# Performance work log

Hardware: AMD Instinct MI355X
Metric: run time of the kernel (lower is better)

## Reference

```python
import jax, jax.numpy as jnp
import numpy as np

NUM_HEADS = 8
HEAD_DIM = 64
D_MODEL = NUM_HEADS * HEAD_DIM  # 512
B, T = 4, 2048


def setup_inputs() -> dict:
    key = jax.random.key(0)
    k1, k2 = jax.random.split(key)
    x = jax.random.normal(k1, (B, T, D_MODEL), dtype=jnp.float32)
    mask = jnp.ones((B, 1, T, T), dtype=jnp.float32)
    W = jax.random.normal(k2, (D_MODEL, 3 * D_MODEL), dtype=jnp.float32) * (D_MODEL ** -0.5)
    b = jnp.zeros((3 * D_MODEL,), dtype=jnp.float32)
    return {"x": x, "mask": mask, "W": W, "b": b}


def reference(x, mask, W, b):
    batch = x.shape[0]
    # fused QKV projection: [B, T, 3D]
    qkv = jnp.einsum("btd,de->bte", x, W) + b
    # NOTE: faithful to torch reshape [B, T, H, Hd, 3] -> the size-3 axis is innermost
    qkv = qkv.reshape(batch, -1, NUM_HEADS, HEAD_DIM, 3)
    qkv = jnp.transpose(qkv, (4, 0, 2, 1, 3))  # [3, B, H, T, Hd]
    q, k, v = qkv[0], qkv[1], qkv[2]
    logits = jnp.einsum("bhqd,bhkd->bhqk", q, k) / (HEAD_DIM ** 0.5)
    logits = logits + (1.0 - mask) * -10000.0
    w = jax.nn.softmax(logits, axis=-1)
    out = jnp.einsum("bhqk,bhkd->bhqd", w, v)  # [B, H, T, Hd]
    out = jnp.transpose(out, (0, 2, 1, 3)).reshape(batch, -1, NUM_HEADS * HEAD_DIM)
    return out
```

## Files before the change

### kernel.cpp

```cpp
#include <hip/hip_runtime.h>
#include <hip/hip_bf16.h>
#include <stdint.h>

#define B_   4
#define T_   2048
#define H_   8
#define HD_  64
#define DM_  512
#define N3_  1536

typedef short bf_el;
typedef __attribute__((ext_vector_type(8))) bf_el bfrag;
typedef __attribute__((ext_vector_type(4))) float ffrag;

#define SCALE_L2E  0.18033688011112043f
#define MASK_L2E   14426.950408889634f

static __device__ __forceinline__ unsigned short f2bf(float f) {
    union { float f; unsigned int i; } v; v.f = f;
    unsigned int r = v.i + 0x7fff + ((v.i >> 16) & 1);
    return (unsigned short)(r >> 16);
}
static __device__ __forceinline__ unsigned short f2bf_fast(float f) {
    union { float f; unsigned int i; } v; v.f = f;
    return (unsigned short)((v.i + 0x8000u) >> 16);
}

__global__ __launch_bounds__(256) void k_prep(const float* __restrict__ W,
                                              const float* __restrict__ X,
                                              const float* __restrict__ mask,
                                              unsigned short* __restrict__ Wt,
                                              unsigned short* __restrict__ Xb,
                                              int* __restrict__ flags) {
    __shared__ __align__(16) unsigned short Ls[64 * 72];
    const int bid = blockIdx.x;
    const int tid = threadIdx.x;

    if (bid < 512) {
        const int R0 = bid * 16;
        const int mb = R0 >> 11;
        const int q0 = R0 & 2047;
        const int e  = mb * 32 + (q0 >> 6);
        const int wave = tid >> 6, lane = tid & 63;
        unsigned int acc = 0u;
        const float* base = mask + (size_t)R0 * T_ + tid * 8;
#pragma unroll
        for (int rr = 0; rr < 16; ++rr) {
            const uint4 u0 = *(const uint4*)(base + (size_t)rr * T_);
            const uint4 u1 = *(const uint4*)(base + (size_t)rr * T_ + 4);
            acc |= (u0.x ^ 0x3F800000u) | (u0.y ^ 0x3F800000u) |
                   (u0.z ^ 0x3F800000u) | (u0.w ^ 0x3F800000u) |
                   (u1.x ^ 0x3F800000u) | (u1.y ^ 0x3F800000u) |
                   (u1.z ^ 0x3F800000u) | (u1.w ^ 0x3F800000u);
        }
        unsigned long long bal = __ballot(acc != 0u);
        if (lane == 0 && bal != 0ULL) {
#pragma unroll
            for (int j = 0; j < 8; ++j)
                if ((bal >> (8 * j)) & 0xFFULL)
                    atomicOr(&flags[e * 32 + wave * 8 + j], 1);
        }
        return;
    }
    if (bid < 768) {
        const int b2 = bid - 512;
        const float* src = X + (size_t)b2 * 16384;
        unsigned short* dst = Xb + (size_t)b2 * 16384;
#pragma unroll
        for (int j = 0; j < 8; ++j) {
            int idx = j * 512 + tid * 2;
            float4 f0 = *(const float4*)(src + idx * 4);
            float4 f1 = *(const float4*)(src + idx * 4 + 4);
            __align__(16) unsigned short t8[8];
            t8[0] = f2bf_fast(f0.x); t8[1] = f2bf_fast(f0.y);
            t8[2] = f2bf_fast(f0.z); t8[3] = f2bf_fast(f0.w);
            t8[4] = f2bf_fast(f1.x); t8[5] = f2bf_fast(f1.y);
            t8[6] = f2bf_fast(f1.z); t8[7] = f2bf_fast(f1.w);
            *(uint4*)(dst + idx * 4) = *(const uint4*)t8;
        }
        return;
    }
    {
        const int t  = bid - 768;
        const int n0 = (t % 24) * 64;
        const int k0 = (t / 24) * 64;
#pragma unroll
        for (int i = 0; i < 4; ++i) {
            int chunk = tid + i * 256;
            int k = chunk >> 4;
            int c = chunk & 15;
            float4 f = *(const float4*)(W + (size_t)(k0 + k) * N3_ + n0 + c * 4);
            unsigned short* p = Ls + k * 72 + c * 4;
            p[0] = f2bf(f.x); p[1] = f2bf(f.y); p[2] = f2bf(f.z); p[3] = f2bf(f.w);
        }
        __syncthreads();
        const int n = tid >> 2;
        const int g = tid & 3;
        __align__(16) unsigned short tmp[16];
#pragma unroll
        for (int i = 0; i < 16; ++i) tmp[i] = Ls[(g * 16 + i) * 72 + n];
        uint4* dst = (uint4*)(Wt + (size_t)(n0 + n) * DM_ + k0 + g * 16);
        dst[0] = *(const uint4*)(tmp);
        dst[1] = *(const uint4*)(tmp + 8);
    }
}

__global__ __launch_bounds__(256) void k_gemm_qkv(const unsigned short* __restrict__ Xb,
                                                  const unsigned short* __restrict__ Wt,
                                                  const float* __restrict__ bias,
                                                  unsigned short* __restrict__ Qb,
                                                  unsigned short* __restrict__ Kb,
                                                  unsigned short* __restrict__ Vtb) {
    __shared__ __align__(16) unsigned short SH[12800];
    unsigned short* As = SH;
    unsigned short* Bs = SH + 5120;
    unsigned short* Cs = SH;

    const int tid  = threadIdx.x;
    const int wave = tid >> 6;
    const int lane = tid & 63;
    const int quad = lane >> 4;
    const int l16  = lane & 15;
    const int wm = wave >> 1, wn = wave & 1;
    const int h  = blockIdx.x >> 6;
    const int m0 = (blockIdx.x & 63) * 128;
    const int n0 = h * 192;

    float bvv[6];
#pragma unroll
    for (int ni = 0; ni < 6; ++ni) bvv[ni] = bias[n0 + wn * 96 + ni * 16 + l16];

    ffrag acc[4][6];
#pragma unroll
    for (int i = 0; i < 4; ++i)
#pragma unroll
        for (int j = 0; j < 6; ++j) acc[i][j] = (ffrag){0.f, 0.f, 0.f, 0.f};

    for (int kt = 0; kt < 16; ++kt) {
        __syncthreads();
#pragma unroll
        for (int i = 0; i < 2; ++i) {
            int chunk = tid + i * 256;
            int r = chunk >> 2, c = chunk & 3;
            *(uint4*)(As + r * 40 + c * 8) =
                *(const uint4*)(Xb + (size_t)(m0 + r) * DM_ + kt * 32 + c * 8);
        }
#pragma unroll
        for (int i = 0; i < 3; ++i) {
            int chunk = tid + i * 256;
            int r = chunk >> 2, c = chunk & 3;
            *(uint4*)(Bs + r * 40 + c * 8) =
                *(const uint4*)(Wt + (size_t)(n0 + r) * DM_ + kt * 32 + c * 8);
        }
        __syncthreads();
        bfrag af[4], bfr[6];
#pragma unroll
        for (int mi = 0; mi < 4; ++mi)
            af[mi] = *(const bfrag*)(As + (wm * 64 + mi * 16 + l16) * 40 + quad * 8);
#pragma unroll
        for (int ni = 0; ni < 6; ++ni)
            bfr[ni] = *(const bfrag*)(Bs + (wn * 96 + ni * 16 + l16) * 40 + quad * 8);
#pragma unroll
        for (int mi = 0; mi < 4; ++mi)
#pragma unroll
            for (int ni = 0; ni < 6; ++ni)
                acc[mi][ni] = __builtin_amdgcn_mfma_f32_16x16x32_bf16(af[mi], bfr[ni], acc[mi][ni], 0, 0, 0);
    }

    const int b   = m0 >> 11;
    const int tb0 = m0 & 2047;
    const size_t bh = (size_t)(b * 8 + h);
    float cscale[6];
#pragma unroll
    for (int ni = 0; ni < 6; ++ni) {
        int c = wn * 96 + ni * 16 + l16;
        cscale[ni] = (c % 3 == 0) ? SCALE_L2E : 1.0f;
    }
#pragma unroll
    for (int half = 0; half < 2; ++half) {
        __syncthreads();
        if (wm == half) {
#pragma unroll
            for (int mi = 0; mi < 4; ++mi)
#pragma unroll
                for (int ni = 0; ni < 6; ++ni)
#pragma unroll
                    for (int reg = 0; reg < 4; ++reg) {
                        int r = mi * 16 + quad * 4 + reg;
                        int c = wn * 96 + ni * 16 + l16;
                        Cs[r * 200 + c] = f2bf_fast((acc[mi][ni][reg] + bvv[ni]) * cscale[ni]);
                    }
        }
        __syncthreads();
        const int tb = tb0 + half * 64;
#pragma unroll
        for (int i = 0; i < 2; ++i) {
            int idx = tid + i * 256;
            int tl = idx >> 3, hc = (idx & 7) * 8;
            __align__(16) unsigned short tq[8], tk[8];
#pragma unroll
            for (int j = 0; j < 8; ++j) {
                tq[j] = Cs[tl * 200 + (hc + j) * 3 + 0];
                tk[j] = Cs[tl * 200 + (hc + j) * 3 + 1];
            }
            *(uint4*)(Qb + (bh * T_ + tb + tl) * HD_ + hc) = *(const uint4*)tq;
            *(uint4*)(Kb + (bh * T_ + tb + tl) * HD_ + hc) = *(const uint4*)tk;
        }
#pragma unroll
        for (int i = 0; i < 2; ++i) {
            int idx = tid + i * 256;
            int hd = idx >> 3, t8 = (idx & 7) * 8;
            __align__(16) unsigned short tv[8];
#pragma unroll
            for (int j = 0; j < 8; ++j)
                tv[j] = Cs[(t8 + j) * 200 + hd * 3 + 2];
            *(uint4*)(Vtb + (bh * HD_ + hd) * T_ + tb + t8) = *(const uint4*)tv;
        }
    }
}

__global__ __launch_bounds__(256) void k_attn(const unsigned short* __restrict__ Q,
                                              const unsigned short* __restrict__ K,
                                              const unsigned short* __restrict__ Vt,
                                              const float* __restrict__ mask,
                                              const int* __restrict__ flags,
                                              float* __restrict__ out) {
    __shared__ __align__(16) unsigned short Ks[2][64 * 72];
    __shared__ __align__(16) unsigned short Vs[2][64 * 72];
    __shared__ __align__(16) unsigned short Ps[4][16 * 72];

    const int tid = threadIdx.x;
    const int wave = tid >> 6, lane = tid & 63;
    const int quad = lane >> 4, l16 = lane & 15;
    const int bh = blockIdx.x & 31, b = bh >> 3, h = bh & 7;
    const int qt = blockIdx.x >> 5;
    const int q0 = qt * 128;

    bfrag qf[2][2];
#pragma unroll
    for (int g = 0; g < 2; ++g) {
        size_t qrow = ((size_t)bh * T_ + q0 + wave * 32 + g * 16 + l16) * HD_;
        qf[g][0] = *(const bfrag*)(Q + qrow + quad * 8);
        qf[g][1] = *(const bfrag*)(Q + qrow + 32 + quad * 8);
    }
    float lsum[2][4] = {{0.f,0.f,0.f,0.f},{0.f,0.f,0.f,0.f}};
    ffrag of[2][4];
#pragma unroll
    for (int g = 0; g < 2; ++g)
#pragma unroll
        for (int nb = 0; nb < 4; ++nb) of[g][nb] = (ffrag){0.f, 0.f, 0.f, 0.f};

    const int fbase0 = (b * 32 + qt * 2) * 32;
    const int fbase1 = (b * 32 + qt * 2 + 1) * 32;

    const int sr0 = tid >> 3, sr1 = (tid + 256) >> 3, sc = tid & 7;
    const unsigned short* Kbase = K  + (size_t)bh * T_ * HD_;
    const unsigned short* Vbase = Vt + (size_t)bh * HD_ * T_;

    uint4 kreg[2], vreg[2];
    kreg[0] = *(const uint4*)(Kbase + (size_t)sr0 * HD_ + sc * 8);
    kreg[1] = *(const uint4*)(Kbase + (size_t)sr1 * HD_ + sc * 8);
    vreg[0] = *(const uint4*)(Vbase + (size_t)sr0 * T_ + sc * 8);
    vreg[1] = *(const uint4*)(Vbase + (size_t)sr1 * T_ + sc * 8);
    *(uint4*)(&Ks[0][sr0 * 72 + sc * 8]) = kreg[0];
    *(uint4*)(&Ks[0][sr1 * 72 + sc * 8]) = kreg[1];
    *(uint4*)(&Vs[0][sr0 * 72 + sc * 8]) = vreg[0];
    *(uint4*)(&Vs[0][sr1 * 72 + sc * 8]) = vreg[1];
    __syncthreads();

    for (int kt = 0; kt < 32; ++kt) {
        const int cur = kt & 1;
        if (kt < 31) {
            const int kn = (kt + 1) * 64;
            kreg[0] = *(const uint4*)(Kbase + (size_t)(kn + sr0) * HD_ + sc * 8);
            kreg[1] = *(const uint4*)(Kbase + (size_t)(kn + sr1) * HD_ + sc * 8);
            vreg[0] = *(const uint4*)(Vbase + (size_t)sr0 * T_ + kn + sc * 8);
            vreg[1] = *(const uint4*)(Vbase + (size_t)sr1 * T_ + kn + sc * 8);
        }
        int fl[2];
        fl[0] = flags[fbase0 + kt];
        fl[1] = flags[fbase1 + kt];

        bfrag vf[2][4];
#pragma unroll
        for (int ks = 0; ks < 2; ++ks)
#pragma unroll
            for (int nb = 0; nb < 4; ++nb)
                vf[ks][nb] = *(const bfrag*)(&Vs[cur][(nb * 16 + l16) * 72 + (ks * 4 + quad) * 8]);

#pragma unroll
        for (int g = 0; g < 2; ++g) {
            ffrag sf[4];
#pragma unroll
            for (int ns = 0; ns < 4; ++ns) {
                ffrag a = (ffrag){0.f, 0.f, 0.f, 0.f};
#pragma unroll
                for (int ks = 0; ks < 2; ++ks) {
                    bfrag kf = *(const bfrag*)(&Ks[cur][(ns * 16 + l16) * 72 + (ks * 4 + quad) * 8]);
                    a = __builtin_amdgcn_mfma_f32_16x16x32_bf16(qf[g][ks], kf, a, 0, 0, 0);
                }
                sf[ns] = a;
            }
            if (fl[g]) {
#pragma unroll
                for (int reg = 0; reg < 4; ++reg) {
                    int tq = q0 + wave * 32 + g * 16 + quad * 4 + reg;
                    const float* mrow = mask + ((size_t)b * T_ + tq) * T_ + kt * 64;
#pragma unroll
                    for (int ns = 0; ns < 4; ++ns) {
                        float msk = mrow[ns * 16 + l16];
                        float p = __builtin_amdgcn_exp2f(
                            fmaf(msk, MASK_L2E, sf[ns][reg] - MASK_L2E));
                        lsum[g][reg] += p;
                        Ps[wave][(quad * 4 + reg) * 72 + ns * 16 + l16] = f2bf_fast(p);
                    }
                }
            } else {
#pragma unroll
                for (int reg = 0; reg < 4; ++reg) {
#pragma unroll
                    for (int ns = 0; ns < 4; ++ns) {
                        float p = __builtin_amdgcn_exp2f(sf[ns][reg]);
                        lsum[g][reg] += p;
                        Ps[wave][(quad * 4 + reg) * 72 + ns * 16 + l16] = f2bf_fast(p);
                    }
                }
            }
#pragma unroll
            for (int ks = 0; ks < 2; ++ks) {
                bfrag pf = *(const bfrag*)(&Ps[wave][l16 * 72 + (ks * 4 + quad) * 8]);
#pragma unroll
                for (int nb = 0; nb < 4; ++nb)
                    of[g][nb] = __builtin_amdgcn_mfma_f32_16x16x32_bf16(pf, vf[ks][nb], of[g][nb], 0, 0, 0);
            }
        }
        if (kt < 31) {
            const int nxt = cur ^ 1;
            *(uint4*)(&Ks[nxt][sr0 * 72 + sc * 8]) = kreg[0];
            *(uint4*)(&Ks[nxt][sr1 * 72 + sc * 8]) = kreg[1];
            *(uint4*)(&Vs[nxt][sr0 * 72 + sc * 8]) = vreg[0];
            *(uint4*)(&Vs[nxt][sr1 * 72 + sc * 8]) = vreg[1];
            __syncthreads();
        }
    }
#pragma unroll
    for (int g = 0; g < 2; ++g)
#pragma unroll
    for (int reg = 0; reg < 4; ++reg) {
        float s = lsum[g][reg];
#pragma unroll
        for (int d = 1; d < 16; d <<= 1) s += __shfl_xor(s, d, 64);
        float inv = 1.0f / s;
        int t = q0 + wave * 32 + g * 16 + quad * 4 + reg;
#pragma unroll
        for (int nb = 0; nb < 4; ++nb)
            out[((size_t)b * T_ + t) * DM_ + h * 64 + nb * 16 + l16] = of[g][nb][reg] * inv;
    }
}

extern "C" void kernel_launch(void* const* d_in, const int* in_sizes, int n_in,
                              void* d_out, int out_size, void* d_ws, size_t ws_size,
                              hipStream_t stream) {
    const float* X    = (const float*)d_in[0];
    const float* mask = (const float*)d_in[1];
    const float* W    = (const float*)d_in[2];
    const float* bias = (const float*)d_in[3];
    float* outp = (float*)d_out;

    char* ws = (char*)d_ws;
    unsigned short* Wt  = (unsigned short*)(ws);
    unsigned short* Xb  = (unsigned short*)(ws + 1572864);
    unsigned short* Qb  = (unsigned short*)(ws + 9961472);
    unsigned short* Kb  = (unsigned short*)(ws + 18350080);
    unsigned short* Vtb = (unsigned short*)(ws + 26738688);
    int*            flg = (int*)(ws + 35127296);

    hipMemsetAsync(flg, 0, 16384, stream);
    k_prep     <<<dim3(960), 256, 0, stream>>>(W, X, mask, Wt, Xb, flg);
    k_gemm_qkv <<<dim3(512), 256, 0, stream>>>(Xb, Wt, bias, Qb, Kb, Vtb);
    k_attn     <<<dim3(512), 256, 0, stream>>>(Qb, Kb, Vtb, mask, flg, outp);
}
```

Measured before the change: 215.8 us.

## Halve QKV GEMM M-tile, register-prefetch operands, drop flag memset via per-part flags

```diff
diff --git a/kernel.cpp b/kernel.cpp
--- a/kernel.cpp
+++ b/kernel.cpp
@@ -31,7 +31,7 @@
                                               const float* __restrict__ mask,
                                               unsigned short* __restrict__ Wt,
                                               unsigned short* __restrict__ Xb,
-                                              int* __restrict__ flags) {
+                                              int* __restrict__ flags4) {
     __shared__ __align__(16) unsigned short Ls[64 * 72];
     const int bid = blockIdx.x;
     const int tid = threadIdx.x;
@@ -41,6 +41,7 @@
         const int mb = R0 >> 11;
         const int q0 = R0 & 2047;
         const int e  = mb * 32 + (q0 >> 6);
+        const int part = (R0 >> 4) & 3;
         const int wave = tid >> 6, lane = tid & 63;
         unsigned int acc = 0u;
         const float* base = mask + (size_t)R0 * T_ + tid * 8;
@@ -54,11 +55,9 @@
                    (u1.z ^ 0x3F800000u) | (u1.w ^ 0x3F800000u);
         }
         unsigned long long bal = __ballot(acc != 0u);
-        if (lane == 0 && bal != 0ULL) {
-#pragma unroll
-            for (int j = 0; j < 8; ++j)
-                if ((bal >> (8 * j)) & 0xFFULL)
-                    atomicOr(&flags[e * 32 + wave * 8 + j], 1);
+        if (lane < 8) {
+            const int kt = wave * 8 + lane;
+            flags4[(e * 32 + kt) * 4 + part] = ((bal >> (8 * lane)) & 0xFFULL) ? 1 : 0;
         }
         return;
     }
@@ -105,15 +104,15 @@
     }
 }
 
-__global__ __launch_bounds__(256) void k_gemm_qkv(const unsigned short* __restrict__ Xb,
-                                                  const unsigned short* __restrict__ Wt,
-                                                  const float* __restrict__ bias,
-                                                  unsigned short* __restrict__ Qb,
-                                                  unsigned short* __restrict__ Kb,
-                                                  unsigned short* __restrict__ Vtb) {
+__global__ __launch_bounds__(256, 4) void k_gemm_qkv(const unsigned short* __restrict__ Xb,
+                                                     const unsigned short* __restrict__ Wt,
+                                                     const float* __restrict__ bias,
+                                                     unsigned short* __restrict__ Qb,
+                                                     unsigned short* __restrict__ Kb,
+                                                     unsigned short* __restrict__ Vtb) {
     __shared__ __align__(16) unsigned short SH[12800];
     unsigned short* As = SH;
-    unsigned short* Bs = SH + 5120;
+    unsigned short* Bs = SH + 2560;
     unsigned short* Cs = SH;
 
     const int tid  = threadIdx.x;
@@ -122,53 +121,60 @@
     const int quad = lane >> 4;
     const int l16  = lane & 15;
     const int wm = wave >> 1, wn = wave & 1;
-    const int h  = blockIdx.x >> 6;
-    const int m0 = (blockIdx.x & 63) * 128;
+    const int h  = blockIdx.x >> 7;
+    const int m0 = (blockIdx.x & 127) * 64;
     const int n0 = h * 192;
 
     float bvv[6];
 #pragma unroll
     for (int ni = 0; ni < 6; ++ni) bvv[ni] = bias[n0 + wn * 96 + ni * 16 + l16];
 
-    ffrag acc[4][6];
-#pragma unroll
-    for (int i = 0; i < 4; ++i)
+    ffrag acc[2][6];
+#pragma unroll
+    for (int i = 0; i < 2; ++i)
 #pragma unroll
         for (int j = 0; j < 6; ++j) acc[i][j] = (ffrag){0.f, 0.f, 0.f, 0.f};
+
+    const int ar = tid >> 2, ac = tid & 3;
+    const int br0 = tid >> 2, br1 = (tid + 256) >> 2, br2 = (tid + 512) >> 2;
+    const int bc  = tid & 3;
+    uint4 pa, pb0, pb1, pb2;
+
+    pa  = *(const uint4*)(Xb + (size_t)(m0 + ar) * DM_ + ac * 8);
+    pb0 = *(const uint4*)(Wt + (size_t)(n0 + br0) * DM_ + bc * 8);
+    pb1 = *(const uint4*)(Wt + (size_t)(n0 + br1) * DM_ + bc * 8);
+    pb2 = *(const uint4*)(Wt + (size_t)(n0 + br2) * DM_ + bc * 8);
 
     for (int kt = 0; kt < 16; ++kt) {
         __syncthreads();
-#pragma unroll
-        for (int i = 0; i < 2; ++i) {
-            int chunk = tid + i * 256;
-            int r = chunk >> 2, c = chunk & 3;
-            *(uint4*)(As + r * 40 + c * 8) =
-                *(const uint4*)(Xb + (size_t)(m0 + r) * DM_ + kt * 32 + c * 8);
-        }
-#pragma unroll
-        for (int i = 0; i < 3; ++i) {
-            int chunk = tid + i * 256;
-            int r = chunk >> 2, c = chunk & 3;
-            *(uint4*)(Bs + r * 40 + c * 8) =
-                *(const uint4*)(Wt + (size_t)(n0 + r) * DM_ + kt * 32 + c * 8);
-        }
+        *(uint4*)(As + ar * 40 + ac * 8)  = pa;
+        *(uint4*)(Bs + br0 * 40 + bc * 8) = pb0;
+        *(uint4*)(Bs + br1 * 40 + bc * 8) = pb1;
+        *(uint4*)(Bs + br2 * 40 + bc * 8) = pb2;
         __syncthreads();
-        bfrag af[4], bfr[6];
-#pragma unroll
-        for (int mi = 0; mi < 4; ++mi)
-            af[mi] = *(const bfrag*)(As + (wm * 64 + mi * 16 + l16) * 40 + quad * 8);
+        if (kt < 15) {
+            const int ko = (kt + 1) * 32;
+            pa  = *(const uint4*)(Xb + (size_t)(m0 + ar) * DM_ + ko + ac * 8);
+            pb0 = *(const uint4*)(Wt + (size_t)(n0 + br0) * DM_ + ko + bc * 8);
+            pb1 = *(const uint4*)(Wt + (size_t)(n0 + br1) * DM_ + ko + bc * 8);
+            pb2 = *(const uint4*)(Wt + (size_t)(n0 + br2) * DM_ + ko + bc * 8);
+        }
+        bfrag af[2], bfr[6];
+#pragma unroll
+        for (int mi = 0; mi < 2; ++mi)
+            af[mi] = *(const bfrag*)(As + (wm * 32 + mi * 16 + l16) * 40 + quad * 8);
 #pragma unroll
         for (int ni = 0; ni < 6; ++ni)
             bfr[ni] = *(const bfrag*)(Bs + (wn * 96 + ni * 16 + l16) * 40 + quad * 8);
 #pragma unroll
-        for (int mi = 0; mi < 4; ++mi)
+        for (int mi = 0; mi < 2; ++mi)
 #pragma unroll
             for (int ni = 0; ni < 6; ++ni)
                 acc[mi][ni] = __builtin_amdgcn_mfma_f32_16x16x32_bf16(af[mi], bfr[ni], acc[mi][ni], 0, 0, 0);
     }
 
-    const int b   = m0 >> 11;
-    const int tb0 = m0 & 2047;
+    const int b  = m0 >> 11;
+    const int tb = m0 & 2047;
     const size_t bh = (size_t)(b * 8 + h);
     float cscale[6];
 #pragma unroll
@@ -176,46 +182,40 @@
         int c = wn * 96 + ni * 16 + l16;
         cscale[ni] = (c % 3 == 0) ? SCALE_L2E : 1.0f;
     }
-#pragma unroll
-    for (int half = 0; half < 2; ++half) {
-        __syncthreads();
-        if (wm == half) {
-#pragma unroll
-            for (int mi = 0; mi < 4; ++mi)
-#pragma unroll
-                for (int ni = 0; ni < 6; ++ni)
-#pragma unroll
-                    for (int reg = 0; reg < 4; ++reg) {
-                        int r = mi * 16 + quad * 4 + reg;
-                        int c = wn * 96 + ni * 16 + l16;
-                        Cs[r * 200 + c] = f2bf_fast((acc[mi][ni][reg] + bvv[ni]) * cscale[ni]);
-                    }
-        }
-        __syncthreads();
-        const int tb = tb0 + half * 64;
-#pragma unroll
-        for (int i = 0; i < 2; ++i) {
-            int idx = tid + i * 256;
-            int tl = idx >> 3, hc = (idx & 7) * 8;
-            __align__(16) unsigned short tq[8], tk[8];
-#pragma unroll
-            for (int j = 0; j < 8; ++j) {
-                tq[j] = Cs[tl * 200 + (hc + j) * 3 + 0];
-                tk[j] = Cs[tl * 200 + (hc + j) * 3 + 1];
+    __syncthreads();
+#pragma unroll
+    for (int mi = 0; mi < 2; ++mi)
+#pragma unroll
+        for (int ni = 0; ni < 6; ++ni)
+#pragma unroll
+            for (int reg = 0; reg < 4; ++reg) {
+                int r = wm * 32 + mi * 16 + quad * 4 + reg;
+                int c = wn * 96 + ni * 16 + l16;
+                Cs[r * 200 + c] = f2bf_fast((acc[mi][ni][reg] + bvv[ni]) * cscale[ni]);
             }
-            *(uint4*)(Qb + (bh * T_ + tb + tl) * HD_ + hc) = *(const uint4*)tq;
-            *(uint4*)(Kb + (bh * T_ + tb + tl) * HD_ + hc) = *(const uint4*)tk;
-        }
-#pragma unroll
-        for (int i = 0; i < 2; ++i) {
-            int idx = tid + i * 256;
-            int hd = idx >> 3, t8 = (idx & 7) * 8;
-            __align__(16) unsigned short tv[8];
-#pragma unroll
-            for (int j = 0; j < 8; ++j)
-                tv[j] = Cs[(t8 + j) * 200 + hd * 3 + 2];
-            *(uint4*)(Vtb + (bh * HD_ + hd) * T_ + tb + t8) = *(const uint4*)tv;
-        }
+    __syncthreads();
+#pragma unroll
+    for (int i = 0; i < 2; ++i) {
+        int idx = tid + i * 256;
+        int tl = idx >> 3, hc = (idx & 7) * 8;
+        __align__(16) unsigned short tq[8], tk[8];
+#pragma unroll
+        for (int j = 0; j < 8; ++j) {
+            tq[j] = Cs[tl * 200 + (hc + j) * 3 + 0];
+            tk[j] = Cs[tl * 200 + (hc + j) * 3 + 1];
+        }
+        *(uint4*)(Qb + (bh * T_ + tb + tl) * HD_ + hc) = *(const uint4*)tq;
+        *(uint4*)(Kb + (bh * T_ + tb + tl) * HD_ + hc) = *(const uint4*)tk;
+    }
+#pragma unroll
+    for (int i = 0; i < 2; ++i) {
+        int idx = tid + i * 256;
+        int hd = idx >> 3, t8 = (idx & 7) * 8;
+        __align__(16) unsigned short tv[8];
+#pragma unroll
+        for (int j = 0; j < 8; ++j)
+            tv[j] = Cs[(t8 + j) * 200 + hd * 3 + 2];
+        *(uint4*)(Vtb + (bh * HD_ + hd) * T_ + tb + t8) = *(const uint4*)tv;
     }
 }
 
@@ -223,7 +223,7 @@
                                               const unsigned short* __restrict__ K,
                                               const unsigned short* __restrict__ Vt,
                                               const float* __restrict__ mask,
-                                              const int* __restrict__ flags,
+                                              const int4* __restrict__ flags4,
                                               float* __restrict__ out) {
     __shared__ __align__(16) unsigned short Ks[2][64 * 72];
     __shared__ __align__(16) unsigned short Vs[2][64 * 72];
@@ -250,8 +250,8 @@
 #pragma unroll
         for (int nb = 0; nb < 4; ++nb) of[g][nb] = (ffrag){0.f, 0.f, 0.f, 0.f};
 
-    const int fbase0 = (b * 32 + qt * 2) * 32;
-    const int fbase1 = (b * 32 + qt * 2 + 1) * 32;
+    const int e0 = b * 32 + qt * 2;
+    const int e1 = e0 + 1;
 
     const int sr0 = tid >> 3, sr1 = (tid + 256) >> 3, sc = tid & 7;
     const unsigned short* Kbase = K  + (size_t)bh * T_ * HD_;
@@ -277,9 +277,11 @@
             vreg[0] = *(const uint4*)(Vbase + (size_t)sr0 * T_ + kn + sc * 8);
             vreg[1] = *(const uint4*)(Vbase + (size_t)sr1 * T_ + kn + sc * 8);
         }
+        int4 F0 = flags4[e0 * 32 + kt];
+        int4 F1 = flags4[e1 * 32 + kt];
         int fl[2];
-        fl[0] = flags[fbase0 + kt];
-        fl[1] = flags[fbase1 + kt];
+        fl[0] = F0.x | F0.y | F0.z | F0.w;
+        fl[1] = F1.x | F1.y | F1.z | F1.w;
 
         bfrag vf[2][4];
 #pragma unroll
@@ -375,8 +377,7 @@
     unsigned short* Vtb = (unsigned short*)(ws + 26738688);
     int*            flg = (int*)(ws + 35127296);
 
-    hipMemsetAsync(flg, 0, 16384, stream);
-    k_prep     <<<dim3(960), 256, 0, stream>>>(W, X, mask, Wt, Xb, flg);
-    k_gemm_qkv <<<dim3(512), 256, 0, stream>>>(Xb, Wt, bias, Qb, Kb, Vtb);
-    k_attn     <<<dim3(512), 256, 0, stream>>>(Qb, Kb, Vtb, mask, flg, outp);
-}
+    k_prep     <<<dim3(960),  256, 0, stream>>>(W, X, mask, Wt, Xb, flg);
+    k_gemm_qkv <<<dim3(1024), 256, 0, stream>>>(Xb, Wt, bias, Qb, Kb, Vtb);
+    k_attn     <<<dim3(512),  256, 0, stream>>>(Qb, Kb, Vtb, mask, (const int4*)flg, outp);
+}
```

Result: no change. 216.9 us (+0.5%).
